# Kernel tuning notes

Measured on AMD Instinct MI355X. Metric: run time of the kernel, lower is better.

## Reference

```python
import math
import jax, jax.numpy as jnp
import numpy as np

N = 50000
C = 128      # in_channels == out_channels
H = 8        # nhead
D = C // H   # head_dim = 16
E = 800000


def _layernorm(x, g, b, eps=1e-5):
    mu = jnp.mean(x, axis=-1, keepdims=True)
    var = jnp.var(x, axis=-1, keepdims=True)
    return (x - mu) * jax.lax.rsqrt(var + eps) * g + b


def setup_inputs() -> dict:
    key = jax.random.key(0)
    ks = jax.random.split(key, 12)
    s = 1.0 / math.sqrt(C)          # ~xavier scale
    s4 = 1.0 / math.sqrt(4 * C)
    return {
        "x": jax.random.normal(ks[0], (N, C), dtype=jnp.float32),
        "edge_index": jax.random.randint(ks[1], (2, E), 0, N, dtype=jnp.int64),
        "Wq": jax.random.normal(ks[2], (C, C), dtype=jnp.float32) * s,
        "Wk": jax.random.normal(ks[3], (C, C), dtype=jnp.float32) * s,
        "Wv": jax.random.normal(ks[4], (C, C), dtype=jnp.float32) * s,
        "Wo": jax.random.normal(ks[5], (C, C), dtype=jnp.float32) * s,
        "bo": jnp.zeros((C,), dtype=jnp.float32),
        "Wf1": jax.random.normal(ks[6], (C, 4 * C), dtype=jnp.float32) * s,
        "bf1": jnp.zeros((4 * C,), dtype=jnp.float32),
        "Wf2": jax.random.normal(ks[7], (4 * C, C), dtype=jnp.float32) * s4,
        "bf2": jnp.zeros((C,), dtype=jnp.float32),
        "g1": jnp.ones((C,), dtype=jnp.float32),
        "b1": jnp.zeros((C,), dtype=jnp.float32),
        "g2": jnp.ones((C,), dtype=jnp.float32),
        "b2": jnp.zeros((C,), dtype=jnp.float32),
    }


def reference(x, edge_index, Wq, Wk, Wv, Wo, bo, Wf1, bf1, Wf2, bf2, g1, b1, g2, b2):
    n = x.shape[0]
    loops = jnp.arange(n, dtype=edge_index.dtype)
    row = jnp.concatenate([edge_index[0], loops])  # source nodes
    col = jnp.concatenate([edge_index[1], loops])  # destination nodes

    q = (x @ Wq).reshape(n, H, D)
    k = (x @ Wk).reshape(n, H, D)
    v = (x @ Wv).reshape(n, H, D)

    # edge-level attention scores [E+N, H]
    scores = jnp.einsum('ehd,ehd->eh', q[row], k[col]) / math.sqrt(D)
    smax = jax.ops.segment_max(scores, col, num_segments=n)  # every node has a self-loop
    exp = jnp.exp(scores - smax[col])
    ssum = jax.ops.segment_sum(exp, col, num_segments=n)
    alpha = exp / (ssum[col] + 1e-8)

    out = jax.ops.segment_sum(v[row] * alpha[..., None], col, num_segments=n)
    attn = out.reshape(n, C) @ Wo + bo

    residual = x  # input_proj is Identity (in_channels == out_channels)
    x1 = _layernorm(residual + attn, g1, b1)
    ffn = jax.nn.gelu(x1 @ Wf1 + bf1, approximate=False) @ Wf2 + bf2
    return _layernorm(x1 + ffn, g2, b2)
```

## Files before the change

kernel.cpp:

```cpp
#include <hip/hip_runtime.h>
#include <cmath>


typedef short bf16x8 __attribute__((ext_vector_type(8)));
typedef float f32x4 __attribute__((ext_vector_type(4)));
typedef unsigned int uint_as1 __attribute__((address_space(1)));
typedef unsigned int uint_as3 __attribute__((address_space(3)));

__device__ inline unsigned short f2bf(float f) {
    unsigned int u = __float_as_uint(f);
    u += 0x7fffu + ((u >> 16) & 1u);
    return (unsigned short)(u >> 16);
}
__device__ inline float bflo(unsigned int w) { return __uint_as_float(w << 16); }
__device__ inline float bfhi(unsigned int w) { return __uint_as_float(w & 0xffff0000u); }

__device__ inline void gload16(const unsigned short* g, unsigned short* l) {
    __builtin_amdgcn_global_load_lds((const uint_as1*)g, (uint_as3*)l, 16, 0, 0);
}

__device__ inline float gelu_f(float x) {
    float ax = fabsf(x) * 0.70710678118f;
    float t = __builtin_amdgcn_rcpf(fmaf(0.3275911f, ax, 1.0f));
    float p = fmaf(1.061405429f, t, -1.453152027f);
    p = fmaf(p, t, 1.421413741f);
    p = fmaf(p, t, -0.284496736f);
    p = fmaf(p, t, 0.254829592f);
    p = p * t;
    float e = __expf(-ax * ax);
    float pe = p * e;
    float w = (x >= 0.f) ? (2.0f - pe) : pe;
    return 0.5f * x * w;
}


__global__ __launch_bounds__(256) void k_init(
    const float* __restrict__ x, unsigned short* __restrict__ xb,
    const float* __restrict__ Wq, const float* __restrict__ Wk,
    const float* __restrict__ Wv, const float* __restrict__ Wo,
    const float* __restrict__ Wf1, const float* __restrict__ Wf2,
    unsigned short* __restrict__ Wqkvt, unsigned short* __restrict__ Wot,
    unsigned short* __restrict__ Wf1t, unsigned short* __restrict__ Wf2t,
    int* __restrict__ cursor, int4* __restrict__ csrz,
    int N, int nCsr4, int nCast) {
    int bid = blockIdx.x;
    int t = threadIdx.x;

    int NBc = (N + 255) >> 8;
    if (bid < NBc) {
        int i = bid * 256 + t;
        if (i < N) cursor[i] = 0;
        return;
    }
    bid -= NBc;
    int NBz = (nCsr4 + 255) >> 8;
    if (bid < NBz) {
        int i = bid * 256 + t;
        if (i < nCsr4) csrz[i] = make_int4(0, 0, 0, 0);
        return;
    }
    bid -= NBz;
    if (bid < nCast) {
        int i = bid * 256 + t;
        if (i < N * 32) {
            float4 v = ((const float4*)x)[i];
            ushort4 o;
            o.x = f2bf(v.x); o.y = f2bf(v.y); o.z = f2bf(v.z); o.w = f2bf(v.w);
            ((ushort4*)xb)[i] = o;
        }
        return;
    }
    bid -= nCast;
    int z, idx;
    if (bid < 256) { z = bid >> 6; idx = (bid & 63) * 256 + t; }
    else           { z = 4 + ((bid - 256) >> 8); idx = ((bid - 256) & 255) * 256 + t; }

    const float* in; unsigned short* out; int K, Co;
    switch (z) {
        case 0: in = Wq;  out = Wqkvt; K = 128; Co = 128; break;
        case 1: in = Wk;  out = Wqkvt; K = 128; Co = 128; break;
        case 2: in = Wv;  out = Wqkvt; K = 128; Co = 128; break;
        case 3: in = Wo;  out = Wot;   K = 128; Co = 128; break;
        case 4: in = Wf1; out = Wf1t;  K = 128; Co = 512; break;
        default: in = Wf2; out = Wf2t; K = 512; Co = 128; break;
    }
    if (idx >= K * Co) return;
    int k = idx / Co, c = idx % Co;
    int row;
    switch (z) {
        case 0: row = ((c >> 1) << 2) | (c & 1); break;
        case 1: row = 256 + c; break;
        case 2: row = (((c >> 1) << 2) | (c & 1)) + 2; break;
        default: row = c; break;
    }
    out[(size_t)row * K + k] = f2bf(in[idx]);
}


__global__ void k_fill(const int* __restrict__ ei, int* __restrict__ cursor,
                       int* __restrict__ csr, int E, int N) {
    int e = blockIdx.x * 256 + threadIdx.x;
    if (e >= E + N) return;
    int row, col;
    if (e < E) { row = ei[e]; col = ei[E + e]; }
    else       { row = col = e - E; }
    int pos = atomicAdd(&cursor[col], 1);
    csr[col * 64 + pos] = row;
}


template <int EPI, int KS, int WR>
__global__ __launch_bounds__(WR * 128) void k_gemm(
    const unsigned short* __restrict__ A, const unsigned short* __restrict__ Bt,
    const float* __restrict__ bias, const float* __restrict__ resid,
    const float* __restrict__ g, const float* __restrict__ b,
    float* __restrict__ outf, unsigned short* __restrict__ outb,
    int M, int Cout) {
    constexpr int K = KS * 32;
    constexpr int NT = WR * 128;
    constexpr int CPR = K / 8;
    constexpr int RPI = NT / CPR;
    constexpr int NITER = 128 / RPI;
    constexpr int ROWS = WR * 64;
    constexpr int SMU = (128 * K > ROWS * 136) ? 128 * K : ROWS * 136;
    __shared__ unsigned short smem[SMU];
    unsigned short* Bs = smem;

    int tid = threadIdx.x;
    int wid = tid >> 6, lane = tid & 63;
    int quad = lane >> 4, l16 = lane & 15;
    int wr = wid >> 1, wc = wid & 1;
    int m0 = blockIdx.x * ROWS;
    int n0 = blockIdx.y * 128;

    const unsigned short* Arow[4];
#pragma unroll
    for (int ti = 0; ti < 4; ++ti) {
        int row = m0 + wr * 64 + ti * 16 + l16;
        if (row > M - 1) row = M - 1;
        Arow[ti] = A + (size_t)row * K + quad * 8;
    }

#define LOADA(buf, kc)                                                        \
    _Pragma("unroll") for (int ti_ = 0; ti_ < 4; ++ti_)                       \
        _Pragma("unroll") for (int j_ = 0; j_ < 4; ++j_)                      \
            buf[ti_][j_] = *(const bf16x8*)(Arow[ti_] + ((kc) + j_) * 32);

    bf16x8 a0[4][4];
    LOADA(a0, 0);
    bf16x8 a1[4][4];
    if constexpr (KS > 4) { LOADA(a1, 4); }

    {
        int srow = tid / CPR;
        int c = tid % CPR;
        int gc = (c & ~7) | ((c & 7) ^ (srow & 7));
        const unsigned short* src = Bt + (size_t)(n0 + srow) * K + gc * 8;
        unsigned short* dst = Bs + tid * 8;
#pragma unroll
        for (int j = 0; j < NITER; ++j)
            gload16(src + (size_t)j * RPI * K, dst + (size_t)j * RPI * K);
    }
    __syncthreads();

    f32x4 acc[4][4];
#pragma unroll
    for (int i = 0; i < 4; ++i)
#pragma unroll
        for (int j = 0; j < 4; ++j) acc[i][j] = {0.f, 0.f, 0.f, 0.f};

#define KCHUNK(buf, kc)                                                       \
    _Pragma("unroll") for (int ks_ = 0; ks_ < 4; ++ks_) {                     \
        bf16x8 bfr[4];                                                        \
        _Pragma("unroll") for (int tj_ = 0; tj_ < 4; ++tj_) {                 \
            int nr = wc * 64 + tj_ * 16 + l16;                                \
            int cidx = ((kc) + ks_) * 4 + quad;                               \
            int slot = (cidx & ~7) | ((cidx & 7) ^ (nr & 7));                 \
            bfr[tj_] = *(const bf16x8*)&Bs[nr * K + slot * 8];                \
        }                                                                     \
        _Pragma("unroll") for (int ti_ = 0; ti_ < 4; ++ti_)                   \
            _Pragma("unroll") for (int tj_ = 0; tj_ < 4; ++tj_)               \
                acc[ti_][tj_] = __builtin_amdgcn_mfma_f32_16x16x32_bf16(      \
                    buf[ti_][ks_], bfr[tj_], acc[ti_][tj_], 0, 0, 0);         \
    }

    KCHUNK(a0, 0);
    if constexpr (KS > 4) {
        LOADA(a0, 8);
        KCHUNK(a1, 4);
        LOADA(a1, 12);
        KCHUNK(a0, 8);
        KCHUNK(a1, 12);
    }
#undef LOADA
#undef KCHUNK

    unsigned short* Ls = smem;

    if constexpr (EPI != 2) {
        __syncthreads();
        float bi[4];
        if constexpr (EPI == 1) {
#pragma unroll
            for (int tj = 0; tj < 4; ++tj) bi[tj] = bias[n0 + wc * 64 + tj * 16 + l16];
        }
#pragma unroll
        for (int ti = 0; ti < 4; ++ti)
#pragma unroll
            for (int tj = 0; tj < 4; ++tj) {
                int c = wc * 64 + tj * 16 + l16;
#pragma unroll
                for (int r = 0; r < 4; ++r) {
                    int rl = wr * 64 + ti * 16 + quad * 4 + r;
                    float v = acc[ti][tj][r];
                    if constexpr (EPI == 1) v = gelu_f(v + bi[tj]);
                    Ls[rl * 136 + c] = f2bf(v);
                }
            }
        __syncthreads();
        int rl = tid >> 1, half = tid & 1;
        int grow = m0 + rl;
        if (grow < M) {
#pragma unroll
            for (int c8 = 0; c8 < 8; ++c8) {
                uint4 v = *(const uint4*)&Ls[rl * 136 + half * 64 + c8 * 8];
                *(uint4*)&outb[(size_t)grow * Cout + n0 + half * 64 + c8 * 8] = v;
            }
        }
    } else {
        __shared__ float pSum[2][ROWS];
        __shared__ float pSq[2][ROWS];
        float bi[4], gv[4], bv[4];
#pragma unroll
        for (int tj = 0; tj < 4; ++tj) {
            int col = wc * 64 + tj * 16 + l16;
            bi[tj] = bias[col]; gv[tj] = g[col]; bv[tj] = b[col];
        }
#pragma unroll
        for (int ti = 0; ti < 4; ++ti)
#pragma unroll
            for (int tj = 0; tj < 4; ++tj) {
                int col = wc * 64 + tj * 16 + l16;
#pragma unroll
                for (int r = 0; r < 4; ++r) {
                    int row = m0 + wr * 64 + ti * 16 + quad * 4 + r;
                    float rv = (row < M) ? resid[(size_t)row * 128 + col] : 0.f;
                    acc[ti][tj][r] += bi[tj] + rv;
                }
            }
#pragma unroll
        for (int ti = 0; ti < 4; ++ti)
#pragma unroll
            for (int r = 0; r < 4; ++r) {
                float s = acc[ti][0][r] + acc[ti][1][r] + acc[ti][2][r] + acc[ti][3][r];
                float q = acc[ti][0][r] * acc[ti][0][r] + acc[ti][1][r] * acc[ti][1][r]
                        + acc[ti][2][r] * acc[ti][2][r] + acc[ti][3][r] * acc[ti][3][r];
                s += __shfl_xor(s, 1); q += __shfl_xor(q, 1);
                s += __shfl_xor(s, 2); q += __shfl_xor(q, 2);
                s += __shfl_xor(s, 4); q += __shfl_xor(q, 4);
                s += __shfl_xor(s, 8); q += __shfl_xor(q, 8);
                if (l16 == 0) {
                    int lr = wr * 64 + ti * 16 + quad * 4 + r;
                    pSum[wc][lr] = s; pSq[wc][lr] = q;
                }
            }
        __syncthreads();
        if (tid < ROWS) {
            float s = pSum[0][tid] + pSum[1][tid];
            float q = pSq[0][tid] + pSq[1][tid];
            float mean = s * 0.0078125f;
            float var = q * 0.0078125f - mean * mean;
            pSum[0][tid] = mean;
            pSq[0][tid] = rsqrtf(var + 1e-5f);
        }
        __syncthreads();
#pragma unroll
        for (int ti = 0; ti < 4; ++ti)
#pragma unroll
            for (int r = 0; r < 4; ++r) {
                int lr = wr * 64 + ti * 16 + quad * 4 + r;
                int row = m0 + lr;
                float mean = pSum[0][lr], rs = pSq[0][lr];
#pragma unroll
                for (int tj = 0; tj < 4; ++tj) {
                    int col = wc * 64 + tj * 16 + l16;
                    float y = (acc[ti][tj][r] - mean) * rs * gv[tj] + bv[tj];
                    if (outf && row < M) outf[(size_t)row * 128 + col] = y;
                    if (outb) Ls[lr * 136 + col] = f2bf(y);
                }
            }
        if (outb) {
            __syncthreads();
            int rl = tid >> 1, half = tid & 1;
            int grow = m0 + rl;
            if (grow < M) {
#pragma unroll
                for (int c8 = 0; c8 < 8; ++c8) {
                    uint4 v = *(const uint4*)&Ls[rl * 136 + half * 64 + c8 * 8];
                    *(uint4*)&outb[(size_t)grow * 128 + half * 64 + c8 * 8] = v;
                }
            }
        }
    }
}


__global__ __launch_bounds__(256) void k_attn(
    const unsigned int* __restrict__ qkv, const int* __restrict__ counts,
    const int* __restrict__ csr, unsigned int* __restrict__ ob, int N) {
    int j = blockIdx.x * 4 + (threadIdx.x >> 6);
    if (j >= N) return;
    int l = threadIdx.x & 63;
    int lk = l & 31;
    int half = l >> 5;
    const uint4* qv4 = (const uint4*)qkv;

    uint2 kw = *(const uint2*)(qkv + (size_t)j * 192 + 128 + lk * 2);
    const float S = 0.36067376022224085f;
    float k0 = bflo(kw.x) * S, k1 = bfhi(kw.x) * S;
    float k2 = bflo(kw.y) * S, k3 = bfhi(kw.y) * S;

    int cnt = counts[j];
    int nb = (cnt + 3) >> 2;
    const int* cp = csr + j * 64;

    int ra0 = cp[half],     rb0 = cp[2 + half];
    int ra1 = cp[4 + half], rb1 = cp[6 + half];
    uint4 gA = qv4[(unsigned)ra0 * 48u + lk];
    uint4 gB = qv4[(unsigned)rb0 * 48u + lk];

    float lsum = 0.f, a0 = 0.f, a1 = 0.f, a2 = 0.f, a3 = 0.f;
    for (int bi = 0; bi < nb; ++bi) {
        int ra2 = cp[(bi + 2) * 4 + half];
        int rb2 = cp[(bi + 2) * 4 + 2 + half];
        uint4 nA = qv4[(unsigned)ra1 * 48u + lk];
        uint4 nB = qv4[(unsigned)rb1 * 48u + lk];

        int rem = cnt - bi * 4;
        {
            float s = fmaf(bflo(gA.x), k0,
                      fmaf(bfhi(gA.x), k1,
                      fmaf(bflo(gA.z), k2, bfhi(gA.z) * k3)));
            s += __shfl_xor(s, 1);
            s += __shfl_xor(s, 2);
            float e = exp2f(s);
            e = (half < rem) ? e : 0.f;
            lsum += e;
            a0 = fmaf(e, bflo(gA.y), a0); a1 = fmaf(e, bfhi(gA.y), a1);
            a2 = fmaf(e, bflo(gA.w), a2); a3 = fmaf(e, bfhi(gA.w), a3);
        }
        {
            float s = fmaf(bflo(gB.x), k0,
                      fmaf(bfhi(gB.x), k1,
                      fmaf(bflo(gB.z), k2, bfhi(gB.z) * k3)));
            s += __shfl_xor(s, 1);
            s += __shfl_xor(s, 2);
            float e = exp2f(s);
            e = (2 + half < rem) ? e : 0.f;
            lsum += e;
            a0 = fmaf(e, bflo(gB.y), a0); a1 = fmaf(e, bfhi(gB.y), a1);
            a2 = fmaf(e, bflo(gB.w), a2); a3 = fmaf(e, bfhi(gB.w), a3);
        }
        gA = nA; gB = nB; ra1 = ra2; rb1 = rb2;
    }

    lsum += __shfl_xor(lsum, 32);
    a0 += __shfl_xor(a0, 32); a1 += __shfl_xor(a1, 32);
    a2 += __shfl_xor(a2, 32); a3 += __shfl_xor(a3, 32);

    if (half == 0) {
        float inv = 1.f / (lsum + 1e-8f);
        uint2 o;
        o.x = ((unsigned int)f2bf(a1 * inv) << 16) | (unsigned int)f2bf(a0 * inv);
        o.y = ((unsigned int)f2bf(a3 * inv) << 16) | (unsigned int)f2bf(a2 * inv);
        *(uint2*)(ob + (size_t)j * 64 + lk * 2) = o;
    }
}


extern "C" void kernel_launch(void* const* d_in, const int* in_sizes, int n_in,
                              void* d_out, int out_size, void* d_ws, size_t ws_size,
                              hipStream_t stream) {
    const float* x   = (const float*)d_in[0];
    const int* ei    = (const int*)d_in[1];
    const float* Wq  = (const float*)d_in[2];
    const float* Wk  = (const float*)d_in[3];
    const float* Wv  = (const float*)d_in[4];
    const float* Wo  = (const float*)d_in[5];
    const float* bo  = (const float*)d_in[6];
    const float* Wf1 = (const float*)d_in[7];
    const float* bf1 = (const float*)d_in[8];
    const float* Wf2 = (const float*)d_in[9];
    const float* bf2 = (const float*)d_in[10];
    const float* g1  = (const float*)d_in[11];
    const float* b1  = (const float*)d_in[12];
    const float* g2  = (const float*)d_in[13];
    const float* b2  = (const float*)d_in[14];

    int N = in_sizes[0] / 128;
    int E = in_sizes[1] / 2;
    int N2 = ((N + 127) / 128) * 128;
    int NE = E + N;

    char* p = (char*)d_ws;
    auto alloc = [&](size_t bytes) -> char* {
        char* r = p;
        p += (bytes + 255) & ~(size_t)255;
        return r;
    };
    unsigned short* qkv = (unsigned short*)alloc((size_t)N2 * 512 * 2);
    unsigned short* ob  = qkv + (size_t)N2 * 384;
    unsigned short* hb  = qkv;
    unsigned short* x1b = (unsigned short*)alloc((size_t)N2 * 128 * 2);
    unsigned short* xb  = x1b;
    float* x1f          = (float*)alloc((size_t)N2 * 128 * 4);
    unsigned short* Wqkvt = (unsigned short*)alloc(384 * 128 * 2);
    unsigned short* Wot   = (unsigned short*)alloc(128 * 128 * 2);
    unsigned short* Wf1t  = (unsigned short*)alloc(512 * 128 * 2);
    unsigned short* Wf2t  = (unsigned short*)alloc(128 * 512 * 2);
    int* cursor = (int*)alloc((size_t)N * 4);
    int* csr    = (int*)alloc(((size_t)N * 64 + 64) * 4);

    int nCsr4 = N * 16 + 16;
    int nCast = (N * 32 + 255) / 256;
    int nInit = ((N + 255) / 256) + ((nCsr4 + 255) / 256) + nCast + 768;
    int M128 = (N + 127) / 128;
    int M256 = (N + 255) / 256;

    k_init<<<nInit, 256, 0, stream>>>(x, xb, Wq, Wk, Wv, Wo, Wf1, Wf2,
                                      Wqkvt, Wot, Wf1t, Wf2t,
                                      cursor, (int4*)csr, N, nCsr4, nCast);
    k_fill<<<(NE + 255) / 256, 256, 0, stream>>>(ei, cursor, csr, E, N);

    k_gemm<0, 4, 2><<<dim3(M128, 3), 256, 0, stream>>>(
        xb, Wqkvt, nullptr, nullptr, nullptr, nullptr, nullptr, qkv, N, 384);

    k_attn<<<(N + 3) / 4, 256, 0, stream>>>((const unsigned int*)qkv, cursor,
                                            csr, (unsigned int*)ob, N);

    k_gemm<2, 4, 2><<<dim3(M128, 1), 256, 0, stream>>>(
        ob, Wot, bo, x, g1, b1, x1f, x1b, N, 128);

    k_gemm<1, 4, 2><<<dim3(M128, 4), 256, 0, stream>>>(
        x1b, Wf1t, bf1, nullptr, nullptr, nullptr, nullptr, hb, N, 512);

    k_gemm<2, 16, 4><<<dim3(M256, 1), 512, 0, stream>>>(
        hb, Wf2t, bf2, x1f, g2, b2, (float*)d_out, nullptr, N, 128);
}
```

Baseline: 342.3 us.

## Fuse output projection, LayerNorms and FFN into one tail kernel; merge fill with QKV GEMM

Replaces the three post-attention GEMM launches with a single per-128-row kernel. It computes the Wo projection, residual plus LayerNorm1, and the FFN in four 128-wide hidden chunks, keeping x1 and the GELU activations in shared memory, then applies LayerNorm2. This removes the HBM round trips for x1 (fp32 and bf16) and the 512-wide hidden tensor. The CSR fill is merged into the QKV GEMM launch, and CSR indices shrink from int to 16-bit. The costs are heavy shared-memory use (about 120KB), which limits occupancy, and the 16-bit indices, which only work while N stays below 65536.

```diff
diff --git a/kernel.cpp b/kernel.cpp
--- a/kernel.cpp
+++ b/kernel.cpp
@@ -34,6 +34,55 @@
 }
 
 
+__device__ __forceinline__ void stage_panel(unsigned short* Bs,
+                                            const unsigned short* base,
+                                            int strideK) {
+    int tid = threadIdx.x;
+    int srow = tid >> 4, cc = tid & 15;
+    int gc = (cc & ~7) | ((cc & 7) ^ (srow & 7));
+    const unsigned short* src = base + (size_t)srow * strideK + gc * 8;
+    unsigned short* dst = Bs + srow * 128 + cc * 8;
+#pragma unroll
+    for (int j = 0; j < 8; ++j)
+        gload16(src + (size_t)j * 16 * strideK, dst + j * 16 * 128);
+}
+
+__device__ __forceinline__ void loadA_g(bf16x8 (&af)[4][4],
+                                        const unsigned short* A, int M,
+                                        int m0, int wr, int l16, int quad) {
+#pragma unroll
+    for (int ti = 0; ti < 4; ++ti) {
+        int row = m0 + wr * 64 + ti * 16 + l16;
+        if (row > M - 1) row = M - 1;
+        const unsigned short* ar = A + (size_t)row * 128 + quad * 8;
+#pragma unroll
+        for (int j = 0; j < 4; ++j) af[ti][j] = *(const bf16x8*)(ar + j * 32);
+    }
+}
+
+__device__ __forceinline__ void mm16(f32x4 (&acc)[4][4], const bf16x8 (&af)[4][4],
+                                     const unsigned short* Bs,
+                                     int wc, int quad, int l16) {
+#pragma unroll
+    for (int ks = 0; ks < 4; ++ks) {
+        bf16x8 bfr[4];
+#pragma unroll
+        for (int tj = 0; tj < 4; ++tj) {
+            int nr = wc * 64 + tj * 16 + l16;
+            int cidx = ks * 4 + quad;
+            int slot = (cidx & ~7) | ((cidx & 7) ^ (nr & 7));
+            bfr[tj] = *(const bf16x8*)&Bs[nr * 128 + slot * 8];
+        }
+#pragma unroll
+        for (int ti = 0; ti < 4; ++ti)
+#pragma unroll
+            for (int tj = 0; tj < 4; ++tj)
+                acc[ti][tj] = __builtin_amdgcn_mfma_f32_16x16x32_bf16(
+                    af[ti][ks], bfr[tj], acc[ti][tj], 0, 0, 0);
+    }
+}
+
+
 __global__ __launch_bounds__(256) void k_init(
     const float* __restrict__ x, unsigned short* __restrict__ xb,
     const float* __restrict__ Wq, const float* __restrict__ Wk,
@@ -97,70 +146,37 @@
 }
 
 
-__global__ void k_fill(const int* __restrict__ ei, int* __restrict__ cursor,
-                       int* __restrict__ csr, int E, int N) {
-    int e = blockIdx.x * 256 + threadIdx.x;
-    if (e >= E + N) return;
-    int row, col;
-    if (e < E) { row = ei[e]; col = ei[E + e]; }
-    else       { row = col = e - E; }
-    int pos = atomicAdd(&cursor[col], 1);
-    csr[col * 64 + pos] = row;
-}
-
-
-template <int EPI, int KS, int WR>
-__global__ __launch_bounds__(WR * 128) void k_gemm(
-    const unsigned short* __restrict__ A, const unsigned short* __restrict__ Bt,
-    const float* __restrict__ bias, const float* __restrict__ resid,
-    const float* __restrict__ g, const float* __restrict__ b,
-    float* __restrict__ outf, unsigned short* __restrict__ outb,
-    int M, int Cout) {
-    constexpr int K = KS * 32;
-    constexpr int NT = WR * 128;
-    constexpr int CPR = K / 8;
-    constexpr int RPI = NT / CPR;
-    constexpr int NITER = 128 / RPI;
-    constexpr int ROWS = WR * 64;
-    constexpr int SMU = (128 * K > ROWS * 136) ? 128 * K : ROWS * 136;
-    __shared__ unsigned short smem[SMU];
-    unsigned short* Bs = smem;
+__global__ __launch_bounds__(256) void k_fq(
+    const int* __restrict__ ei, int* __restrict__ cursor,
+    unsigned short* __restrict__ csr, int E, int N,
+    const unsigned short* __restrict__ xb, const unsigned short* __restrict__ Wqkvt,
+    unsigned short* __restrict__ qkv, int nFillB, int Mt) {
+    __shared__ unsigned short smem[128 * 136];
+
+    if ((int)blockIdx.x < nFillB) {
+        int e = blockIdx.x * 256 + threadIdx.x;
+        if (e < E + N) {
+            int row, col;
+            if (e < E) { row = ei[e]; col = ei[E + e]; }
+            else       { row = col = e - E; }
+            int pos = atomicAdd(&cursor[col], 1);
+            csr[(size_t)col * 64 + pos] = (unsigned short)row;
+        }
+        return;
+    }
+
+    int bid = blockIdx.x - nFillB;
+    int z = bid / Mt, mt = bid % Mt;
+    int m0 = mt * 128, n0 = z * 128;
 
     int tid = threadIdx.x;
     int wid = tid >> 6, lane = tid & 63;
     int quad = lane >> 4, l16 = lane & 15;
     int wr = wid >> 1, wc = wid & 1;
-    int m0 = blockIdx.x * ROWS;
-    int n0 = blockIdx.y * 128;
-
-    const unsigned short* Arow[4];
-#pragma unroll
-    for (int ti = 0; ti < 4; ++ti) {
-        int row = m0 + wr * 64 + ti * 16 + l16;
-        if (row > M - 1) row = M - 1;
-        Arow[ti] = A + (size_t)row * K + quad * 8;
-    }
-
-#define LOADA(buf, kc)                                                        \
-    _Pragma("unroll") for (int ti_ = 0; ti_ < 4; ++ti_)                       \
-        _Pragma("unroll") for (int j_ = 0; j_ < 4; ++j_)                      \
-            buf[ti_][j_] = *(const bf16x8*)(Arow[ti_] + ((kc) + j_) * 32);
-
-    bf16x8 a0[4][4];
-    LOADA(a0, 0);
-    bf16x8 a1[4][4];
-    if constexpr (KS > 4) { LOADA(a1, 4); }
-
-    {
-        int srow = tid / CPR;
-        int c = tid % CPR;
-        int gc = (c & ~7) | ((c & 7) ^ (srow & 7));
-        const unsigned short* src = Bt + (size_t)(n0 + srow) * K + gc * 8;
-        unsigned short* dst = Bs + tid * 8;
-#pragma unroll
-        for (int j = 0; j < NITER; ++j)
-            gload16(src + (size_t)j * RPI * K, dst + (size_t)j * RPI * K);
-    }
+
+    bf16x8 af[4][4];
+    loadA_g(af, xb, N, m0, wr, l16, quad);
+    stage_panel(smem, Wqkvt + (size_t)n0 * 128, 128);
     __syncthreads();
 
     f32x4 acc[4][4];
@@ -168,138 +184,28 @@
     for (int i = 0; i < 4; ++i)
 #pragma unroll
         for (int j = 0; j < 4; ++j) acc[i][j] = {0.f, 0.f, 0.f, 0.f};
-
-#define KCHUNK(buf, kc)                                                       \
-    _Pragma("unroll") for (int ks_ = 0; ks_ < 4; ++ks_) {                     \
-        bf16x8 bfr[4];                                                        \
-        _Pragma("unroll") for (int tj_ = 0; tj_ < 4; ++tj_) {                 \
-            int nr = wc * 64 + tj_ * 16 + l16;                                \
-            int cidx = ((kc) + ks_) * 4 + quad;                               \
-            int slot = (cidx & ~7) | ((cidx & 7) ^ (nr & 7));                 \
-            bfr[tj_] = *(const bf16x8*)&Bs[nr * K + slot * 8];                \
-        }                                                                     \
-        _Pragma("unroll") for (int ti_ = 0; ti_ < 4; ++ti_)                   \
-            _Pragma("unroll") for (int tj_ = 0; tj_ < 4; ++tj_)               \
-                acc[ti_][tj_] = __builtin_amdgcn_mfma_f32_16x16x32_bf16(      \
-                    buf[ti_][ks_], bfr[tj_], acc[ti_][tj_], 0, 0, 0);         \
-    }
-
-    KCHUNK(a0, 0);
-    if constexpr (KS > 4) {
-        LOADA(a0, 8);
-        KCHUNK(a1, 4);
-        LOADA(a1, 12);
-        KCHUNK(a0, 8);
-        KCHUNK(a1, 12);
-    }
-#undef LOADA
-#undef KCHUNK
-
-    unsigned short* Ls = smem;
-
-    if constexpr (EPI != 2) {
-        __syncthreads();
-        float bi[4];
-        if constexpr (EPI == 1) {
-#pragma unroll
-            for (int tj = 0; tj < 4; ++tj) bi[tj] = bias[n0 + wc * 64 + tj * 16 + l16];
-        }
-#pragma unroll
-        for (int ti = 0; ti < 4; ++ti)
-#pragma unroll
-            for (int tj = 0; tj < 4; ++tj) {
-                int c = wc * 64 + tj * 16 + l16;
-#pragma unroll
-                for (int r = 0; r < 4; ++r) {
-                    int rl = wr * 64 + ti * 16 + quad * 4 + r;
-                    float v = acc[ti][tj][r];
-                    if constexpr (EPI == 1) v = gelu_f(v + bi[tj]);
-                    Ls[rl * 136 + c] = f2bf(v);
-                }
-            }
-        __syncthreads();
-        int rl = tid >> 1, half = tid & 1;
-        int grow = m0 + rl;
-        if (grow < M) {
-#pragma unroll
-            for (int c8 = 0; c8 < 8; ++c8) {
-                uint4 v = *(const uint4*)&Ls[rl * 136 + half * 64 + c8 * 8];
-                *(uint4*)&outb[(size_t)grow * Cout + n0 + half * 64 + c8 * 8] = v;
-            }
-        }
-    } else {
-        __shared__ float pSum[2][ROWS];
-        __shared__ float pSq[2][ROWS];
-        float bi[4], gv[4], bv[4];
+    mm16(acc, af, smem, wc, quad, l16);
+
+    __syncthreads();
+#pragma unroll
+    for (int ti = 0; ti < 4; ++ti)
 #pragma unroll
         for (int tj = 0; tj < 4; ++tj) {
-            int col = wc * 64 + tj * 16 + l16;
-            bi[tj] = bias[col]; gv[tj] = g[col]; bv[tj] = b[col];
-        }
-#pragma unroll
-        for (int ti = 0; ti < 4; ++ti)
-#pragma unroll
-            for (int tj = 0; tj < 4; ++tj) {
-                int col = wc * 64 + tj * 16 + l16;
-#pragma unroll
-                for (int r = 0; r < 4; ++r) {
-                    int row = m0 + wr * 64 + ti * 16 + quad * 4 + r;
-                    float rv = (row < M) ? resid[(size_t)row * 128 + col] : 0.f;
-                    acc[ti][tj][r] += bi[tj] + rv;
-                }
-            }
-#pragma unroll
-        for (int ti = 0; ti < 4; ++ti)
+            int c = wc * 64 + tj * 16 + l16;
 #pragma unroll
             for (int r = 0; r < 4; ++r) {
-                float s = acc[ti][0][r] + acc[ti][1][r] + acc[ti][2][r] + acc[ti][3][r];
-                float q = acc[ti][0][r] * acc[ti][0][r] + acc[ti][1][r] * acc[ti][1][r]
-                        + acc[ti][2][r] * acc[ti][2][r] + acc[ti][3][r] * acc[ti][3][r];
-                s += __shfl_xor(s, 1); q += __shfl_xor(q, 1);
-                s += __shfl_xor(s, 2); q += __shfl_xor(q, 2);
-                s += __shfl_xor(s, 4); q += __shfl_xor(q, 4);
-                s += __shfl_xor(s, 8); q += __shfl_xor(q, 8);
-                if (l16 == 0) {
-                    int lr = wr * 64 + ti * 16 + quad * 4 + r;
-                    pSum[wc][lr] = s; pSq[wc][lr] = q;
-                }
-            }
-        __syncthreads();
-        if (tid < ROWS) {
-            float s = pSum[0][tid] + pSum[1][tid];
-            float q = pSq[0][tid] + pSq[1][tid];
-            float mean = s * 0.0078125f;
-            float var = q * 0.0078125f - mean * mean;
-            pSum[0][tid] = mean;
-            pSq[0][tid] = rsqrtf(var + 1e-5f);
-        }
-        __syncthreads();
-#pragma unroll
-        for (int ti = 0; ti < 4; ++ti)
-#pragma unroll
-            for (int r = 0; r < 4; ++r) {
-                int lr = wr * 64 + ti * 16 + quad * 4 + r;
-                int row = m0 + lr;
-                float mean = pSum[0][lr], rs = pSq[0][lr];
-#pragma unroll
-                for (int tj = 0; tj < 4; ++tj) {
-                    int col = wc * 64 + tj * 16 + l16;
-                    float y = (acc[ti][tj][r] - mean) * rs * gv[tj] + bv[tj];
-                    if (outf && row < M) outf[(size_t)row * 128 + col] = y;
-                    if (outb) Ls[lr * 136 + col] = f2bf(y);
-                }
-            }
-        if (outb) {
-            __syncthreads();
-            int rl = tid >> 1, half = tid & 1;
-            int grow = m0 + rl;
-            if (grow < M) {
-#pragma unroll
-                for (int c8 = 0; c8 < 8; ++c8) {
-                    uint4 v = *(const uint4*)&Ls[rl * 136 + half * 64 + c8 * 8];
-                    *(uint4*)&outb[(size_t)grow * 128 + half * 64 + c8 * 8] = v;
-                }
-            }
+                int rl = wr * 64 + ti * 16 + quad * 4 + r;
+                smem[rl * 136 + c] = f2bf(acc[ti][tj][r]);
+            }
+        }
+    __syncthreads();
+    int rl = tid >> 1, half = tid & 1;
+    int grow = m0 + rl;
+    if (grow < N) {
+#pragma unroll
+        for (int c8 = 0; c8 < 8; ++c8) {
+            uint4 v = *(const uint4*)&smem[rl * 136 + half * 64 + c8 * 8];
+            *(uint4*)&qkv[(size_t)grow * 384 + n0 + half * 64 + c8 * 8] = v;
         }
     }
 }
@@ -307,7 +213,8 @@
 
 __global__ __launch_bounds__(256) void k_attn(
     const unsigned int* __restrict__ qkv, const int* __restrict__ counts,
-    const int* __restrict__ csr, unsigned int* __restrict__ ob, int N) {
+    const unsigned short* __restrict__ csr, unsigned int* __restrict__ ob,
+    int N) {
     int j = blockIdx.x * 4 + (threadIdx.x >> 6);
     if (j >= N) return;
     int l = threadIdx.x & 63;
@@ -322,7 +229,7 @@
 
     int cnt = counts[j];
     int nb = (cnt + 3) >> 2;
-    const int* cp = csr + j * 64;
+    const unsigned short* cp = csr + (size_t)j * 64;
 
     int ra0 = cp[half],     rb0 = cp[2 + half];
     int ra1 = cp[4 + half], rb1 = cp[6 + half];
@@ -375,6 +282,213 @@
         o.y = ((unsigned int)f2bf(a3 * inv) << 16) | (unsigned int)f2bf(a2 * inv);
         *(uint2*)(ob + (size_t)j * 64 + lk * 2) = o;
     }
+}
+
+
+__global__ __launch_bounds__(256) void k_tail(
+    const unsigned short* __restrict__ ob, const unsigned short* __restrict__ Wot,
+    const float* __restrict__ bo, const float* __restrict__ x,
+    const float* __restrict__ g1, const float* __restrict__ b1,
+    const unsigned short* __restrict__ Wf1t, const float* __restrict__ bf1,
+    const unsigned short* __restrict__ Wf2t, const float* __restrict__ bf2,
+    const float* __restrict__ g2, const float* __restrict__ b2,
+    float* __restrict__ dout, int M) {
+    __shared__ unsigned short Bs[128 * 128];
+    __shared__ unsigned short Ls[128 * 136];
+    __shared__ float X1[128 * 132];
+    __shared__ float pS[2][128], pQ[2][128];
+
+    int tid = threadIdx.x;
+    int wid = tid >> 6, lane = tid & 63;
+    int quad = lane >> 4, l16 = lane & 15;
+    int wr = wid >> 1, wc = wid & 1;
+    int m0 = blockIdx.x * 128;
+
+    float gv1[4], bv1[4], gv2[4], bv2[4], bi[4];
+#pragma unroll
+    for (int tj = 0; tj < 4; ++tj) {
+        int col = wc * 64 + tj * 16 + l16;
+        gv1[tj] = g1[col]; bv1[tj] = b1[col];
+        gv2[tj] = g2[col]; bv2[tj] = b2[col];
+        bi[tj] = bo[col];
+    }
+
+    {
+        bf16x8 af[4][4];
+        loadA_g(af, ob, M, m0, wr, l16, quad);
+        stage_panel(Bs, Wot, 128);
+        __syncthreads();
+
+        f32x4 acc[4][4];
+#pragma unroll
+        for (int i = 0; i < 4; ++i)
+#pragma unroll
+            for (int j = 0; j < 4; ++j) acc[i][j] = {0.f, 0.f, 0.f, 0.f};
+        mm16(acc, af, Bs, wc, quad, l16);
+
+#pragma unroll
+        for (int ti = 0; ti < 4; ++ti)
+#pragma unroll
+            for (int tj = 0; tj < 4; ++tj) {
+                int col = wc * 64 + tj * 16 + l16;
+#pragma unroll
+                for (int r = 0; r < 4; ++r) {
+                    int row = m0 + wr * 64 + ti * 16 + quad * 4 + r;
+                    float rv = (row < M) ? x[(size_t)row * 128 + col] : 0.f;
+                    acc[ti][tj][r] += bi[tj] + rv;
+                }
+            }
+#pragma unroll
+        for (int ti = 0; ti < 4; ++ti)
+#pragma unroll
+            for (int r = 0; r < 4; ++r) {
+                float s = acc[ti][0][r] + acc[ti][1][r] + acc[ti][2][r] + acc[ti][3][r];
+                float q = acc[ti][0][r] * acc[ti][0][r] + acc[ti][1][r] * acc[ti][1][r]
+                        + acc[ti][2][r] * acc[ti][2][r] + acc[ti][3][r] * acc[ti][3][r];
+                s += __shfl_xor(s, 1); q += __shfl_xor(q, 1);
+                s += __shfl_xor(s, 2); q += __shfl_xor(q, 2);
+                s += __shfl_xor(s, 4); q += __shfl_xor(q, 4);
+                s += __shfl_xor(s, 8); q += __shfl_xor(q, 8);
+                if (l16 == 0) {
+                    int lr = wr * 64 + ti * 16 + quad * 4 + r;
+                    pS[wc][lr] = s; pQ[wc][lr] = q;
+                }
+            }
+        __syncthreads();
+        if (tid < 128) {
+            float s = pS[0][tid] + pS[1][tid];
+            float q = pQ[0][tid] + pQ[1][tid];
+            float mean = s * 0.0078125f;
+            float var = q * 0.0078125f - mean * mean;
+            pS[0][tid] = mean;
+            pQ[0][tid] = rsqrtf(var + 1e-5f);
+        }
+        __syncthreads();
+#pragma unroll
+        for (int ti = 0; ti < 4; ++ti)
+#pragma unroll
+            for (int r = 0; r < 4; ++r) {
+                int lr = wr * 64 + ti * 16 + quad * 4 + r;
+                float mean = pS[0][lr], rs = pQ[0][lr];
+#pragma unroll
+                for (int tj = 0; tj < 4; ++tj) {
+                    int col = wc * 64 + tj * 16 + l16;
+                    float y = (acc[ti][tj][r] - mean) * rs * gv1[tj] + bv1[tj];
+                    X1[lr * 132 + col] = y;
+                    Ls[lr * 136 + col] = f2bf(y);
+                }
+            }
+    }
+    __syncthreads();
+
+    bf16x8 ax1[4][4];
+#pragma unroll
+    for (int ti = 0; ti < 4; ++ti) {
+        int rl = wr * 64 + ti * 16 + l16;
+#pragma unroll
+        for (int j = 0; j < 4; ++j)
+            ax1[ti][j] = *(const bf16x8*)&Ls[rl * 136 + j * 32 + quad * 8];
+    }
+
+    f32x4 dacc[4][4];
+#pragma unroll
+    for (int i = 0; i < 4; ++i)
+#pragma unroll
+        for (int j = 0; j < 4; ++j) dacc[i][j] = {0.f, 0.f, 0.f, 0.f};
+
+    for (int c = 0; c < 4; ++c) {
+        __syncthreads();
+        stage_panel(Bs, Wf1t + (size_t)c * 128 * 128, 128);
+        __syncthreads();
+
+        f32x4 hacc[4][4];
+#pragma unroll
+        for (int i = 0; i < 4; ++i)
+#pragma unroll
+            for (int j = 0; j < 4; ++j) hacc[i][j] = {0.f, 0.f, 0.f, 0.f};
+        mm16(hacc, ax1, Bs, wc, quad, l16);
+
+#pragma unroll
+        for (int ti = 0; ti < 4; ++ti)
+#pragma unroll
+            for (int tj = 0; tj < 4; ++tj) {
+                float bb = bf1[c * 128 + wc * 64 + tj * 16 + l16];
+#pragma unroll
+                for (int r = 0; r < 4; ++r) {
+                    int rl = wr * 64 + ti * 16 + quad * 4 + r;
+                    Ls[rl * 136 + wc * 64 + tj * 16 + l16] =
+                        f2bf(gelu_f(hacc[ti][tj][r] + bb));
+                }
+            }
+        __syncthreads();
+
+        bf16x8 ah[4][4];
+#pragma unroll
+        for (int ti = 0; ti < 4; ++ti) {
+            int rl = wr * 64 + ti * 16 + l16;
+#pragma unroll
+            for (int j = 0; j < 4; ++j)
+                ah[ti][j] = *(const bf16x8*)&Ls[rl * 136 + j * 32 + quad * 8];
+        }
+        __syncthreads();
+        stage_panel(Bs, Wf2t + (size_t)c * 128, 512);
+        __syncthreads();
+        mm16(dacc, ah, Bs, wc, quad, l16);
+    }
+
+#pragma unroll
+    for (int ti = 0; ti < 4; ++ti)
+#pragma unroll
+        for (int tj = 0; tj < 4; ++tj) {
+            int col = wc * 64 + tj * 16 + l16;
+            float bb = bf2[col];
+#pragma unroll
+            for (int r = 0; r < 4; ++r) {
+                int lr = wr * 64 + ti * 16 + quad * 4 + r;
+                dacc[ti][tj][r] += bb + X1[lr * 132 + col];
+            }
+        }
+#pragma unroll
+    for (int ti = 0; ti < 4; ++ti)
+#pragma unroll
+        for (int r = 0; r < 4; ++r) {
+            float s = dacc[ti][0][r] + dacc[ti][1][r] + dacc[ti][2][r] + dacc[ti][3][r];
+            float q = dacc[ti][0][r] * dacc[ti][0][r] + dacc[ti][1][r] * dacc[ti][1][r]
+                    + dacc[ti][2][r] * dacc[ti][2][r] + dacc[ti][3][r] * dacc[ti][3][r];
+            s += __shfl_xor(s, 1); q += __shfl_xor(q, 1);
+            s += __shfl_xor(s, 2); q += __shfl_xor(q, 2);
+            s += __shfl_xor(s, 4); q += __shfl_xor(q, 4);
+            s += __shfl_xor(s, 8); q += __shfl_xor(q, 8);
+            if (l16 == 0) {
+                int lr = wr * 64 + ti * 16 + quad * 4 + r;
+                pS[wc][lr] = s; pQ[wc][lr] = q;
+            }
+        }
+    __syncthreads();
+    if (tid < 128) {
+        float s = pS[0][tid] + pS[1][tid];
+        float q = pQ[0][tid] + pQ[1][tid];
+        float mean = s * 0.0078125f;
+        float var = q * 0.0078125f - mean * mean;
+        pS[0][tid] = mean;
+        pQ[0][tid] = rsqrtf(var + 1e-5f);
+    }
+    __syncthreads();
+#pragma unroll
+    for (int ti = 0; ti < 4; ++ti)
+#pragma unroll
+        for (int r = 0; r < 4; ++r) {
+            int lr = wr * 64 + ti * 16 + quad * 4 + r;
+            int row = m0 + lr;
+            if (row >= M) continue;
+            float mean = pS[0][lr], rs = pQ[0][lr];
+#pragma unroll
+            for (int tj = 0; tj < 4; ++tj) {
+                int col = wc * 64 + tj * 16 + l16;
+                dout[(size_t)row * 128 + col] =
+                    (dacc[ti][tj][r] - mean) * rs * gv2[tj] + bv2[tj];
+            }
+        }
 }
 
 
@@ -408,42 +522,33 @@
         p += (bytes + 255) & ~(size_t)255;
         return r;
     };
-    unsigned short* qkv = (unsigned short*)alloc((size_t)N2 * 512 * 2);
-    unsigned short* ob  = qkv + (size_t)N2 * 384;
-    unsigned short* hb  = qkv;
-    unsigned short* x1b = (unsigned short*)alloc((size_t)N2 * 128 * 2);
-    unsigned short* xb  = x1b;
-    float* x1f          = (float*)alloc((size_t)N2 * 128 * 4);
+    unsigned short* qkv = (unsigned short*)alloc((size_t)N2 * 384 * 2);
+    unsigned short* ob  = (unsigned short*)alloc((size_t)N2 * 128 * 2);
+    unsigned short* xb  = (unsigned short*)alloc((size_t)N2 * 128 * 2);
     unsigned short* Wqkvt = (unsigned short*)alloc(384 * 128 * 2);
     unsigned short* Wot   = (unsigned short*)alloc(128 * 128 * 2);
     unsigned short* Wf1t  = (unsigned short*)alloc(512 * 128 * 2);
     unsigned short* Wf2t  = (unsigned short*)alloc(128 * 512 * 2);
     int* cursor = (int*)alloc((size_t)N * 4);
-    int* csr    = (int*)alloc(((size_t)N * 64 + 64) * 4);
-
-    int nCsr4 = N * 16 + 16;
+    unsigned short* csr = (unsigned short*)alloc(((size_t)N * 64 + 256) * 2);
+
+    int nCsr4 = N * 8 + 32;
     int nCast = (N * 32 + 255) / 256;
     int nInit = ((N + 255) / 256) + ((nCsr4 + 255) / 256) + nCast + 768;
     int M128 = (N + 127) / 128;
-    int M256 = (N + 255) / 256;
+    int nFillB = (NE + 255) / 256;
 
     k_init<<<nInit, 256, 0, stream>>>(x, xb, Wq, Wk, Wv, Wo, Wf1, Wf2,
                                       Wqkvt, Wot, Wf1t, Wf2t,
                                       cursor, (int4*)csr, N, nCsr4, nCast);
-    k_fill<<<(NE + 255) / 256, 256, 0, stream>>>(ei, cursor, csr, E, N);
-
-    k_gemm<0, 4, 2><<<dim3(M128, 3), 256, 0, stream>>>(
-        xb, Wqkvt, nullptr, nullptr, nullptr, nullptr, nullptr, qkv, N, 384);
+
+    k_fq<<<nFillB + 3 * M128, 256, 0, stream>>>(ei, cursor, csr, E, N,
+                                                xb, Wqkvt, qkv, nFillB, M128);
 
     k_attn<<<(N + 3) / 4, 256, 0, stream>>>((const unsigned int*)qkv, cursor,
                                             csr, (unsigned int*)ob, N);
 
-    k_gemm<2, 4, 2><<<dim3(M128, 1), 256, 0, stream>>>(
-        ob, Wot, bo, x, g1, b1, x1f, x1b, N, 128);
-
-    k_gemm<1, 4, 2><<<dim3(M128, 4), 256, 0, stream>>>(
-        x1b, Wf1t, bf1, nullptr, nullptr, nullptr, nullptr, hb, N, 512);
-
-    k_gemm<2, 16, 4><<<dim3(M256, 1), 512, 0, stream>>>(
-        hb, Wf2t, bf2, x1f, g2, b2, (float*)d_out, nullptr, N, 128);
-}
+    k_tail<<<M128, 256, 0, stream>>>(ob, Wot, bo, x, g1, b1,
+                                     Wf1t, bf1, Wf2t, bf2, g2, b2,
+                                     (float*)d_out, N);
+}
```

Result: slower. 349.2 us (+2.0%).

## Unify GEMM into K-tiled 128x128 kernel, shrink CSR to u16, stage fp32 LN stores

Applied to the files above, without the earlier changes.

Replaces the templated GEMM with one kernel that loops over 128-wide K panels, staging each B panel in a fixed 128x136 LDS buffer. The final FFN GEMM now uses 256-thread 128-row tiles instead of 512-thread 256-row tiles. The fp32 layernorm output is staged through LDS so global stores are coalesced float4 writes. The CSR neighbor list is stored as 16-bit indices, halving its memory traffic, but this only works while N fits in 65536. The K loop syncs twice per panel and does not overlap the global loads with MFMA work.

```diff
diff --git a/kernel.cpp b/kernel.cpp
--- a/kernel.cpp
+++ b/kernel.cpp
@@ -34,6 +34,55 @@
 }
 
 
+__device__ __forceinline__ void stage_panel(unsigned short* Bs,
+                                            const unsigned short* base,
+                                            int strideK) {
+    int tid = threadIdx.x;
+    int srow = tid >> 4, cc = tid & 15;
+    int gc = (cc & ~7) | ((cc & 7) ^ (srow & 7));
+    const unsigned short* src = base + (size_t)srow * strideK + gc * 8;
+    unsigned short* dst = Bs + srow * 128 + cc * 8;
+#pragma unroll
+    for (int j = 0; j < 8; ++j)
+        gload16(src + (size_t)j * 16 * strideK, dst + j * 16 * 128);
+}
+
+__device__ __forceinline__ void loadA_k(bf16x8 (&af)[4][4],
+                                        const unsigned short* A, int M, int K,
+                                        int m0, int ko, int wr, int l16, int quad) {
+#pragma unroll
+    for (int ti = 0; ti < 4; ++ti) {
+        int row = m0 + wr * 64 + ti * 16 + l16;
+        if (row > M - 1) row = M - 1;
+        const unsigned short* ar = A + (size_t)row * K + ko + quad * 8;
+#pragma unroll
+        for (int j = 0; j < 4; ++j) af[ti][j] = *(const bf16x8*)(ar + j * 32);
+    }
+}
+
+__device__ __forceinline__ void mm16(f32x4 (&acc)[4][4], const bf16x8 (&af)[4][4],
+                                     const unsigned short* Bs,
+                                     int wc, int quad, int l16) {
+#pragma unroll
+    for (int ks = 0; ks < 4; ++ks) {
+        bf16x8 bfr[4];
+#pragma unroll
+        for (int tj = 0; tj < 4; ++tj) {
+            int nr = wc * 64 + tj * 16 + l16;
+            int cidx = ks * 4 + quad;
+            int slot = (cidx & ~7) | ((cidx & 7) ^ (nr & 7));
+            bfr[tj] = *(const bf16x8*)&Bs[nr * 128 + slot * 8];
+        }
+#pragma unroll
+        for (int ti = 0; ti < 4; ++ti)
+#pragma unroll
+            for (int tj = 0; tj < 4; ++tj)
+                acc[ti][tj] = __builtin_amdgcn_mfma_f32_16x16x32_bf16(
+                    af[ti][ks], bfr[tj], acc[ti][tj], 0, 0, 0);
+    }
+}
+
+
 __global__ __launch_bounds__(256) void k_init(
     const float* __restrict__ x, unsigned short* __restrict__ xb,
     const float* __restrict__ Wq, const float* __restrict__ Wk,
@@ -98,107 +147,53 @@
 
 
 __global__ void k_fill(const int* __restrict__ ei, int* __restrict__ cursor,
-                       int* __restrict__ csr, int E, int N) {
+                       unsigned short* __restrict__ csr, int E, int N) {
     int e = blockIdx.x * 256 + threadIdx.x;
     if (e >= E + N) return;
     int row, col;
     if (e < E) { row = ei[e]; col = ei[E + e]; }
     else       { row = col = e - E; }
     int pos = atomicAdd(&cursor[col], 1);
-    csr[col * 64 + pos] = row;
-}
-
-
-template <int EPI, int KS, int WR>
-__global__ __launch_bounds__(WR * 128) void k_gemm(
+    csr[(size_t)col * 64 + pos] = (unsigned short)row;
+}
+
+
+template <int EPI, int KT>
+__global__ __launch_bounds__(256) void k_gemm(
     const unsigned short* __restrict__ A, const unsigned short* __restrict__ Bt,
     const float* __restrict__ bias, const float* __restrict__ resid,
     const float* __restrict__ g, const float* __restrict__ b,
     float* __restrict__ outf, unsigned short* __restrict__ outb,
     int M, int Cout) {
-    constexpr int K = KS * 32;
-    constexpr int NT = WR * 128;
-    constexpr int CPR = K / 8;
-    constexpr int RPI = NT / CPR;
-    constexpr int NITER = 128 / RPI;
-    constexpr int ROWS = WR * 64;
-    constexpr int SMU = (128 * K > ROWS * 136) ? 128 * K : ROWS * 136;
-    __shared__ unsigned short smem[SMU];
-    unsigned short* Bs = smem;
+    constexpr int K = KT * 128;
+    __shared__ unsigned short smem[128 * 136];
+    __shared__ float pS[2][128], pQ[2][128];
+    float* LsF = (float*)smem;
 
     int tid = threadIdx.x;
     int wid = tid >> 6, lane = tid & 63;
     int quad = lane >> 4, l16 = lane & 15;
     int wr = wid >> 1, wc = wid & 1;
-    int m0 = blockIdx.x * ROWS;
+    int m0 = blockIdx.x * 128;
     int n0 = blockIdx.y * 128;
 
-    const unsigned short* Arow[4];
-#pragma unroll
-    for (int ti = 0; ti < 4; ++ti) {
-        int row = m0 + wr * 64 + ti * 16 + l16;
-        if (row > M - 1) row = M - 1;
-        Arow[ti] = A + (size_t)row * K + quad * 8;
-    }
-
-#define LOADA(buf, kc)                                                        \
-    _Pragma("unroll") for (int ti_ = 0; ti_ < 4; ++ti_)                       \
-        _Pragma("unroll") for (int j_ = 0; j_ < 4; ++j_)                      \
-            buf[ti_][j_] = *(const bf16x8*)(Arow[ti_] + ((kc) + j_) * 32);
-
-    bf16x8 a0[4][4];
-    LOADA(a0, 0);
-    bf16x8 a1[4][4];
-    if constexpr (KS > 4) { LOADA(a1, 4); }
-
-    {
-        int srow = tid / CPR;
-        int c = tid % CPR;
-        int gc = (c & ~7) | ((c & 7) ^ (srow & 7));
-        const unsigned short* src = Bt + (size_t)(n0 + srow) * K + gc * 8;
-        unsigned short* dst = Bs + tid * 8;
-#pragma unroll
-        for (int j = 0; j < NITER; ++j)
-            gload16(src + (size_t)j * RPI * K, dst + (size_t)j * RPI * K);
-    }
-    __syncthreads();
-
     f32x4 acc[4][4];
 #pragma unroll
     for (int i = 0; i < 4; ++i)
 #pragma unroll
         for (int j = 0; j < 4; ++j) acc[i][j] = {0.f, 0.f, 0.f, 0.f};
 
-#define KCHUNK(buf, kc)                                                       \
-    _Pragma("unroll") for (int ks_ = 0; ks_ < 4; ++ks_) {                     \
-        bf16x8 bfr[4];                                                        \
-        _Pragma("unroll") for (int tj_ = 0; tj_ < 4; ++tj_) {                 \
-            int nr = wc * 64 + tj_ * 16 + l16;                                \
-            int cidx = ((kc) + ks_) * 4 + quad;                               \
-            int slot = (cidx & ~7) | ((cidx & 7) ^ (nr & 7));                 \
-            bfr[tj_] = *(const bf16x8*)&Bs[nr * K + slot * 8];                \
-        }                                                                     \
-        _Pragma("unroll") for (int ti_ = 0; ti_ < 4; ++ti_)                   \
-            _Pragma("unroll") for (int tj_ = 0; tj_ < 4; ++tj_)               \
-                acc[ti_][tj_] = __builtin_amdgcn_mfma_f32_16x16x32_bf16(      \
-                    buf[ti_][ks_], bfr[tj_], acc[ti_][tj_], 0, 0, 0);         \
-    }
-
-    KCHUNK(a0, 0);
-    if constexpr (KS > 4) {
-        LOADA(a0, 8);
-        KCHUNK(a1, 4);
-        LOADA(a1, 12);
-        KCHUNK(a0, 8);
-        KCHUNK(a1, 12);
-    }
-#undef LOADA
-#undef KCHUNK
-
-    unsigned short* Ls = smem;
+#pragma unroll
+    for (int kt = 0; kt < KT; ++kt) {
+        bf16x8 af[4][4];
+        loadA_k(af, A, M, K, m0, kt * 128, wr, l16, quad);
+        stage_panel(smem, Bt + (size_t)n0 * K + kt * 128, K);
+        __syncthreads();
+        mm16(acc, af, smem, wc, quad, l16);
+        __syncthreads();
+    }
 
     if constexpr (EPI != 2) {
-        __syncthreads();
         float bi[4];
         if constexpr (EPI == 1) {
 #pragma unroll
@@ -214,22 +209,21 @@
                     int rl = wr * 64 + ti * 16 + quad * 4 + r;
                     float v = acc[ti][tj][r];
                     if constexpr (EPI == 1) v = gelu_f(v + bi[tj]);
-                    Ls[rl * 136 + c] = f2bf(v);
+                    smem[rl * 136 + c] = f2bf(v);
                 }
             }
         __syncthreads();
-        int rl = tid >> 1, half = tid & 1;
-        int grow = m0 + rl;
-        if (grow < M) {
-#pragma unroll
-            for (int c8 = 0; c8 < 8; ++c8) {
-                uint4 v = *(const uint4*)&Ls[rl * 136 + half * 64 + c8 * 8];
-                *(uint4*)&outb[(size_t)grow * Cout + n0 + half * 64 + c8 * 8] = v;
+        int ch = tid & 15;
+#pragma unroll
+        for (int s = 0; s < 8; ++s) {
+            int rl = s * 16 + (tid >> 4);
+            int grow = m0 + rl;
+            if (grow < M) {
+                uint4 v = *(const uint4*)&smem[rl * 136 + ch * 8];
+                *(uint4*)&outb[(size_t)grow * Cout + n0 + ch * 8] = v;
             }
         }
     } else {
-        __shared__ float pSum[2][ROWS];
-        __shared__ float pSq[2][ROWS];
         float bi[4], gv[4], bv[4];
 #pragma unroll
         for (int tj = 0; tj < 4; ++tj) {
@@ -261,43 +255,75 @@
                 s += __shfl_xor(s, 8); q += __shfl_xor(q, 8);
                 if (l16 == 0) {
                     int lr = wr * 64 + ti * 16 + quad * 4 + r;
-                    pSum[wc][lr] = s; pSq[wc][lr] = q;
+                    pS[wc][lr] = s; pQ[wc][lr] = q;
                 }
             }
         __syncthreads();
-        if (tid < ROWS) {
-            float s = pSum[0][tid] + pSum[1][tid];
-            float q = pSq[0][tid] + pSq[1][tid];
+        if (tid < 128) {
+            float s = pS[0][tid] + pS[1][tid];
+            float q = pQ[0][tid] + pQ[1][tid];
             float mean = s * 0.0078125f;
             float var = q * 0.0078125f - mean * mean;
-            pSum[0][tid] = mean;
-            pSq[0][tid] = rsqrtf(var + 1e-5f);
+            pS[0][tid] = mean;
+            pQ[0][tid] = rsqrtf(var + 1e-5f);
         }
         __syncthreads();
-#pragma unroll
-        for (int ti = 0; ti < 4; ++ti)
-#pragma unroll
-            for (int r = 0; r < 4; ++r) {
-                int lr = wr * 64 + ti * 16 + quad * 4 + r;
-                int row = m0 + lr;
-                float mean = pSum[0][lr], rs = pSq[0][lr];
-#pragma unroll
-                for (int tj = 0; tj < 4; ++tj) {
-                    int col = wc * 64 + tj * 16 + l16;
-                    float y = (acc[ti][tj][r] - mean) * rs * gv[tj] + bv[tj];
-                    if (outf && row < M) outf[(size_t)row * 128 + col] = y;
-                    if (outb) Ls[lr * 136 + col] = f2bf(y);
-                }
-            }
+
         if (outb) {
+#pragma unroll
+            for (int ti = 0; ti < 4; ++ti)
+#pragma unroll
+                for (int r = 0; r < 4; ++r) {
+                    int lr = wr * 64 + ti * 16 + quad * 4 + r;
+                    float mean = pS[0][lr], rs = pQ[0][lr];
+#pragma unroll
+                    for (int tj = 0; tj < 4; ++tj) {
+                        int col = wc * 64 + tj * 16 + l16;
+                        smem[lr * 136 + col] =
+                            f2bf((acc[ti][tj][r] - mean) * rs * gv[tj] + bv[tj]);
+                    }
+                }
             __syncthreads();
-            int rl = tid >> 1, half = tid & 1;
-            int grow = m0 + rl;
-            if (grow < M) {
-#pragma unroll
-                for (int c8 = 0; c8 < 8; ++c8) {
-                    uint4 v = *(const uint4*)&Ls[rl * 136 + half * 64 + c8 * 8];
-                    *(uint4*)&outb[(size_t)grow * 128 + half * 64 + c8 * 8] = v;
+            int ch = tid & 15;
+#pragma unroll
+            for (int s = 0; s < 8; ++s) {
+                int rl = s * 16 + (tid >> 4);
+                int grow = m0 + rl;
+                if (grow < M) {
+                    uint4 v = *(const uint4*)&smem[rl * 136 + ch * 8];
+                    *(uint4*)&outb[(size_t)grow * 128 + ch * 8] = v;
+                }
+            }
+        }
+        if (outf) {
+#pragma unroll
+            for (int p = 0; p < 2; ++p) {
+                __syncthreads();
+                if (wr == p) {
+#pragma unroll
+                    for (int ti = 0; ti < 4; ++ti)
+#pragma unroll
+                        for (int r = 0; r < 4; ++r) {
+                            int lr = wr * 64 + ti * 16 + quad * 4 + r;
+                            float mean = pS[0][lr], rs = pQ[0][lr];
+#pragma unroll
+                            for (int tj = 0; tj < 4; ++tj) {
+                                int col = wc * 64 + tj * 16 + l16;
+                                LsF[(lr - p * 64) * 128 + col] =
+                                    (acc[ti][tj][r] - mean) * rs * gv[tj] + bv[tj];
+                            }
+                        }
+                }
+                __syncthreads();
+                int ch = tid & 31;
+#pragma unroll
+                for (int s = 0; s < 8; ++s) {
+                    int rl = s * 8 + (tid >> 5);
+                    int grow = m0 + p * 64 + rl;
+                    if (grow < M) {
+                        float4 v = *(const float4*)&LsF[rl * 128 + ch * 4];
+                        *(float4*)&outf[(size_t)grow * 128 + ch * 4] = v;
+                    }
                 }
             }
         }
@@ -307,7 +333,8 @@
 
 __global__ __launch_bounds__(256) void k_attn(
     const unsigned int* __restrict__ qkv, const int* __restrict__ counts,
-    const int* __restrict__ csr, unsigned int* __restrict__ ob, int N) {
+    const unsigned short* __restrict__ csr, unsigned int* __restrict__ ob,
+    int N) {
     int j = blockIdx.x * 4 + (threadIdx.x >> 6);
     if (j >= N) return;
     int l = threadIdx.x & 63;
@@ -322,7 +349,7 @@
 
     int cnt = counts[j];
     int nb = (cnt + 3) >> 2;
-    const int* cp = csr + j * 64;
+    const unsigned short* cp = csr + (size_t)j * 64;
 
     int ra0 = cp[half],     rb0 = cp[2 + half];
     int ra1 = cp[4 + half], rb1 = cp[6 + half];
@@ -419,31 +446,30 @@
     unsigned short* Wf1t  = (unsigned short*)alloc(512 * 128 * 2);
     unsigned short* Wf2t  = (unsigned short*)alloc(128 * 512 * 2);
     int* cursor = (int*)alloc((size_t)N * 4);
-    int* csr    = (int*)alloc(((size_t)N * 64 + 64) * 4);
-
-    int nCsr4 = N * 16 + 16;
+    unsigned short* csr = (unsigned short*)alloc(((size_t)N * 64 + 256) * 2);
+
+    int nCsr4 = N * 8 + 32;
     int nCast = (N * 32 + 255) / 256;
     int nInit = ((N + 255) / 256) + ((nCsr4 + 255) / 256) + nCast + 768;
     int M128 = (N + 127) / 128;
-    int M256 = (N + 255) / 256;
 
     k_init<<<nInit, 256, 0, stream>>>(x, xb, Wq, Wk, Wv, Wo, Wf1, Wf2,
                                       Wqkvt, Wot, Wf1t, Wf2t,
                                       cursor, (int4*)csr, N, nCsr4, nCast);
     k_fill<<<(NE + 255) / 256, 256, 0, stream>>>(ei, cursor, csr, E, N);
 
-    k_gemm<0, 4, 2><<<dim3(M128, 3), 256, 0, stream>>>(
+    k_gemm<0, 1><<<dim3(M128, 3), 256, 0, stream>>>(
         xb, Wqkvt, nullptr, nullptr, nullptr, nullptr, nullptr, qkv, N, 384);
 
     k_attn<<<(N + 3) / 4, 256, 0, stream>>>((const unsigned int*)qkv, cursor,
                                             csr, (unsigned int*)ob, N);
 
-    k_gemm<2, 4, 2><<<dim3(M128, 1), 256, 0, stream>>>(
+    k_gemm<2, 1><<<dim3(M128, 1), 256, 0, stream>>>(
         ob, Wot, bo, x, g1, b1, x1f, x1b, N, 128);
 
-    k_gemm<1, 4, 2><<<dim3(M128, 4), 256, 0, stream>>>(
+    k_gemm<1, 1><<<dim3(M128, 4), 256, 0, stream>>>(
         x1b, Wf1t, bf1, nullptr, nullptr, nullptr, nullptr, hb, N, 512);
 
-    k_gemm<2, 16, 4><<<dim3(M256, 1), 512, 0, stream>>>(
+    k_gemm<2, 4><<<dim3(M128, 1), 256, 0, stream>>>(
         hb, Wf2t, bf2, x1f, g2, b2, (float*)d_out, nullptr, N, 128);
 }
```

Result: faster. 320.9 us (-6.3%).
